# Kernel optimization log

Measured on AMD Instinct MI355X. Metric: run time of the kernel, lower is better.

The kernel has to match this reference:

```python
import jax, jax.numpy as jnp
import numpy as np
import math

VOCAB, E, CTX, DK, DH, H, HID, L = 50257, 768, 2048, 64, 64, 12, 3072, 2
B, S = 2, 2048
NEG_INF = -1e30


def _pos_encoding(seq_len, dim):
    pos = jnp.arange(seq_len, dtype=jnp.float32)[:, None]
    i = jnp.arange(dim, dtype=jnp.float32)[None, :]
    angle = pos / jnp.power(10000.0, 2.0 * i / dim)
    return jnp.where(jnp.arange(dim)[None, :] % 2 == 0, jnp.sin(angle), jnp.cos(angle))


def _layernorm(x, scale, bias, eps=1e-5):
    mu = jnp.mean(x, axis=-1, keepdims=True)
    var = jnp.var(x, axis=-1, keepdims=True)
    return (x - mu) * jax.lax.rsqrt(var + eps) * scale + bias


def setup_inputs() -> dict:
    key = jax.random.key(0)
    ks = jax.random.split(key, 10)
    s = 0.02  # init scale for stability
    return {
        "tokens": jax.random.randint(ks[0], (B, S), 0, VOCAB),
        "emb": jax.random.normal(ks[1], (VOCAB, E), jnp.float32) * s,
        "ln1_s": jnp.ones((L, E), jnp.float32),
        "ln1_b": jnp.zeros((L, E), jnp.float32),
        "Wq": jax.random.normal(ks[2], (L, H, E, DK), jnp.float32) * s,
        "bq": jnp.zeros((L, H, DK), jnp.float32),
        "Wk": jax.random.normal(ks[3], (L, H, E, DK), jnp.float32) * s,
        "bk": jnp.zeros((L, H, DK), jnp.float32),
        "Wv": jax.random.normal(ks[4], (L, H, E, DH), jnp.float32) * s,
        "bv": jnp.zeros((L, H, DH), jnp.float32),
        "ln2_s": jnp.ones((L, E), jnp.float32),
        "ln2_b": jnp.zeros((L, E), jnp.float32),
        "W1": jax.random.normal(ks[5], (L, E, HID), jnp.float32) * s,
        "b1": jnp.zeros((L, HID), jnp.float32),
        "W2": jax.random.normal(ks[6], (L, HID, E), jnp.float32) * s,
        "b2": jnp.zeros((L, E), jnp.float32),
        "Wout": jax.random.normal(ks[7], (E, VOCAB), jnp.float32) * s,
        "bout": jnp.zeros((VOCAB,), jnp.float32),
    }


def reference(tokens, emb, ln1_s, ln1_b, Wq, bq, Wk, bk, Wv, bv, ln2_s, ln2_b, W1, b1, W2, b2, Wout, bout):
    seq = tokens.shape[1]
    x = emb[tokens] + _pos_encoding(seq, E)  # [B,S,E]
    causal = jnp.triu(jnp.full((seq, seq), NEG_INF, jnp.float32), k=1)
    for l in range(Wq.shape[0]):
        # pre-norm on attention input; note residual adds to the NORMALIZED h (faithful to original)
        h = _layernorm(x, ln1_s[l], ln1_b[l])
        q = jnp.einsum('bse,hed->bhsd', h, Wq[l]) + bq[l][None, :, None, :]
        k = jnp.einsum('bse,hed->bhsd', h, Wk[l]) + bk[l][None, :, None, :]
        v = jnp.einsum('bse,hed->bhsd', h, Wv[l]) + bv[l][None, :, None, :]
        scores = jnp.einsum('bhsd,bhtd->bhst', q, k) / math.sqrt(DK) + causal
        w = jax.nn.softmax(scores, axis=-1)  # [B,H,S,S]
        o = jnp.einsum('bhst,bhtd->bhsd', w, v)  # [B,H,S,DH]
        o = jnp.transpose(o, (0, 2, 1, 3)).reshape(o.shape[0], seq, H * DH)  # concat heads
        x = h + o
        h2 = _layernorm(x, ln2_s[l], ln2_b[l])
        x = h2 + jnp.einsum('bsf,fe->bse', jax.nn.relu(jnp.einsum('bse,ef->bsf', h2, W1[l]) + b1[l]), W2[l]) + b2[l]
    logits = jnp.einsum('bse,ev->bsv', x, Wout) + bout  # training-mode output
    return logits
```

## Files before the change

kernel.cpp:

```cpp
#include <hip/hip_runtime.h>
#include <stdint.h>

#define DEV static __device__ __forceinline__

typedef unsigned short u16;
typedef __attribute__((ext_vector_type(8))) short short8;
typedef __attribute__((ext_vector_type(4))) float f32x4;

#define B_     2
#define S_     2048
#define E_     768
#define H_     12
#define L_     2
#define HID_   3072
#define VOCAB_ 50257
#define VPAD_  50432
#define M_     4096
#define NQKV_  2304

DEV u16 f2bf(float f) {
  union { float f; unsigned u; } x; x.f = f;
  unsigned r = x.u + 0x7fffu + ((x.u >> 16) & 1u);
  return (u16)(r >> 16);
}

DEV void gload16(const void* g, void* lds) {
  __builtin_amdgcn_global_load_lds(
      (const __attribute__((address_space(1))) unsigned int*)g,
      (__attribute__((address_space(3))) unsigned int*)lds, 16, 0, 0);
}

__global__ __launch_bounds__(256) void k_transp(
    const float* __restrict__ in, u16* __restrict__ out,
    int R, int Cin, long long ib1, long long ib2, long long ob1, long long ob2, int zdiv)
{
  __shared__ float t[32][33];
  const int z = blockIdx.z;
  const float* ib = in  + (size_t)(z / zdiv) * ib1 + (size_t)(z % zdiv) * ib2;
  u16*         ob = out + (size_t)(z / zdiv) * ob1 + (size_t)(z % zdiv) * ob2;
  const int c0 = blockIdx.x * 32, r0 = blockIdx.y * 32;
  const int tx = threadIdx.x, ty = threadIdx.y;
#pragma unroll
  for (int i = 0; i < 4; i++) {
    const int c = c0 + tx, r = r0 + ty + i * 8;
    t[ty + i * 8][tx] = (c < Cin) ? ib[(size_t)r * Cin + c] : 0.f;
  }
  __syncthreads();
#pragma unroll
  for (int i = 0; i < 4; i++) {
    const int orow = c0 + ty + i * 8;
    ob[(size_t)orow * R + r0 + tx] = f2bf(t[tx][ty + i * 8]);
  }
}

__global__ __launch_bounds__(256) void k_pack_bias(
    const float* __restrict__ bq, const float* __restrict__ bk,
    const float* __restrict__ bv, float* __restrict__ bqkv)
{
  const int i = blockIdx.x * 256 + threadIdx.x;
  if (i >= L_ * NQKV_) return;
  const int l = i / NQKV_, n = i % NQKV_;
  const float* s = (n < 768) ? bq : (n < 1536) ? bk : bv;
  bqkv[i] = s[l * 768 + (n % 768)];
}

__global__ __launch_bounds__(256) void k_embed(
    const int* __restrict__ tok, const float* __restrict__ emb, float* __restrict__ x)
{
  const int idx = blockIdx.x * 256 + threadIdx.x;
  const int e = idx % E_;
  const int row = idx / E_;
  const int s = row & (S_ - 1);
  const int t = tok[row];
  const float ang = (float)s * expf((float)e * (-2.0f / 768.f) * 9.210340371976184f);
  const float pe = (e & 1) ? cosf(ang) : sinf(ang);
  x[idx] = emb[(size_t)t * E_ + e] + pe;
}

__global__ __launch_bounds__(256) void k_ln(
    const float* __restrict__ xin, const float* __restrict__ sc,
    const float* __restrict__ bi, float* __restrict__ hout, u16* __restrict__ hb)
{
  const int row  = blockIdx.x * 4 + (threadIdx.x >> 6);
  const int lane = threadIdx.x & 63;
  const float* xr = xin + (size_t)row * E_;
  float v[12];
  float s = 0.f;
#pragma unroll
  for (int i = 0; i < 12; i++) { v[i] = xr[i * 64 + lane]; s += v[i]; }
#pragma unroll
  for (int o = 1; o < 64; o <<= 1) s += __shfl_xor(s, o);
  const float mu = s * (1.f / 768.f);
  float s2 = 0.f;
#pragma unroll
  for (int i = 0; i < 12; i++) { const float d = v[i] - mu; s2 += d * d; }
#pragma unroll
  for (int o = 1; o < 64; o <<= 1) s2 += __shfl_xor(s2, o);
  const float rs = rsqrtf(s2 * (1.f / 768.f) + 1e-5f);
#pragma unroll
  for (int i = 0; i < 12; i++) {
    const int c = i * 64 + lane;
    const float ov = (v[i] - mu) * rs * sc[c] + bi[c];
    hout[(size_t)row * E_ + c] = ov;
    hb[(size_t)row * E_ + c]   = f2bf(ov);
  }
}

template <int EPI>
__global__ __launch_bounds__(256) void k_gemm(
    const u16* __restrict__ A, const u16* __restrict__ Bt,
    const float* __restrict__ bias, const float* __restrict__ res,
    void* __restrict__ outp, u16* __restrict__ out2, int Mm, int Nn, int Kk)
{
  __shared__ __align__(16) u16 As[128 * 32];
  __shared__ __align__(16) u16 Bs[128 * 32];
  const int tid  = threadIdx.x;
  const int lane = tid & 63;
  const int wid  = tid >> 6;
  const int wr = wid >> 1, wc = wid & 1;
  const int m0 = blockIdx.y * 128, n0 = blockIdx.x * 128;

  const u16* Ab = A  + (size_t)m0 * Kk;
  const u16* Bb = Bt + (size_t)n0 * Kk;

  f32x4 acc[4][4];
#pragma unroll
  for (int i = 0; i < 4; i++)
#pragma unroll
    for (int j = 0; j < 4; j++) acc[i][j] = (f32x4){0.f, 0.f, 0.f, 0.f};

  const int c0 = tid, c1 = 256 + tid;
  const int a0row = c0 >> 2, a0k = (c0 & 3) * 8;
  const int a1row = c1 >> 2, a1k = (c1 & 3) * 8;
  const int nk = Kk >> 5;
  const int kg = (lane >> 4) * 8;
  const int arow = wr * 64 + (lane & 15);
  const int brow = wc * 64 + (lane & 15);

  for (int kt = 0; kt < nk; ++kt) {
    const int kof = kt * 32;
    __syncthreads();
    gload16(Ab + (size_t)a0row * Kk + kof + a0k, &As[c0 * 8]);
    gload16(Ab + (size_t)a1row * Kk + kof + a1k, &As[c1 * 8]);
    gload16(Bb + (size_t)a0row * Kk + kof + a0k, &Bs[c0 * 8]);
    gload16(Bb + (size_t)a1row * Kk + kof + a1k, &Bs[c1 * 8]);
    asm volatile("s_waitcnt vmcnt(0)" ::: "memory");
    __syncthreads();
    short8 af[4], bf[4];
#pragma unroll
    for (int i = 0; i < 4; i++) af[i] = *(const short8*)&As[(arow + i * 16) * 32 + kg];
#pragma unroll
    for (int i = 0; i < 4; i++) bf[i] = *(const short8*)&Bs[(brow + i * 16) * 32 + kg];
#pragma unroll
    for (int mi = 0; mi < 4; mi++)
#pragma unroll
      for (int ni = 0; ni < 4; ni++)
        acc[mi][ni] = __builtin_amdgcn_mfma_f32_16x16x32_bf16(af[mi], bf[ni], acc[mi][ni], 0, 0, 0);
  }

  const int colg = lane & 15;
  const int rowg = (lane >> 4) * 4;
#pragma unroll
  for (int mi = 0; mi < 4; mi++) {
#pragma unroll
    for (int ni = 0; ni < 4; ni++) {
      const int col = n0 + wc * 64 + ni * 16 + colg;
      const float bb = bias[col];
#pragma unroll
      for (int r = 0; r < 4; r++) {
        const int row = m0 + wr * 64 + mi * 16 + rowg + r;
        float v = acc[mi][ni][r] + bb;
        if (EPI == 0)      ((u16*)outp)[(size_t)row * Nn + col] = f2bf(v);
        else if (EPI == 1) ((u16*)outp)[(size_t)row * Nn + col] = f2bf(fmaxf(v, 0.f));
        else if (EPI == 2) ((float*)outp)[(size_t)row * Nn + col] = v + res[(size_t)row * Nn + col];
        else if (EPI == 4) {
          const float o = v + res[(size_t)row * Nn + col];
          ((float*)outp)[(size_t)row * Nn + col] = o;
          out2[(size_t)row * Nn + col] = f2bf(o);
        }
      }
    }
  }
}

__global__ __launch_bounds__(512, 2) void k_gemm256(
    const u16* __restrict__ A, const u16* __restrict__ Bt,
    const float* __restrict__ bias, float* __restrict__ out,
    int Nn, int Kk, int nreal, int mpx)
{
  __shared__ __align__(16) u16 As[2][256 * 64];
  __shared__ __align__(16) u16 Bs[2][256 * 64];

  const int id = blockIdx.x;
  const int xcd = id & 7;
  const int j = id >> 3;
  const int m0 = (xcd * mpx + (j % mpx)) * 256;
  const int n0 = (j / mpx) * 256;

  const int tid = threadIdx.x, lane = tid & 63, w = tid >> 6;
  const int wr = w >> 2, wcn = w & 3;
  const int l15 = lane & 15, ks = lane >> 4;

  const u16* Ab = A  + (size_t)m0 * Kk;
  const u16* Bb = Bt + (size_t)n0 * Kk;

  const int srow  = lane >> 3;
  const int sslot = ((lane & 7) ^ srow) * 8;
  const int wrow  = w * 8;

  f32x4 acc[8][4];
#pragma unroll
  for (int i = 0; i < 8; i++)
#pragma unroll
    for (int n = 0; n < 4; n++) acc[i][n] = (f32x4){0.f, 0.f, 0.f, 0.f};

  const int nk = Kk >> 6;

  auto stage = [&](int b, int ko) {
    gload16(Ab + (size_t)(wrow + srow) * Kk + ko + sslot,       &As[b][wrow * 64]);
    gload16(Ab + (size_t)(64 + wrow + srow) * Kk + ko + sslot,  &As[b][(64 + wrow) * 64]);
    gload16(Ab + (size_t)(128 + wrow + srow) * Kk + ko + sslot, &As[b][(128 + wrow) * 64]);
    gload16(Ab + (size_t)(192 + wrow + srow) * Kk + ko + sslot, &As[b][(192 + wrow) * 64]);
    gload16(Bb + (size_t)(wrow + srow) * Kk + ko + sslot,       &Bs[b][wrow * 64]);
    gload16(Bb + (size_t)(64 + wrow + srow) * Kk + ko + sslot,  &Bs[b][(64 + wrow) * 64]);
    gload16(Bb + (size_t)(128 + wrow + srow) * Kk + ko + sslot, &Bs[b][(128 + wrow) * 64]);
    gload16(Bb + (size_t)(192 + wrow + srow) * Kk + ko + sslot, &Bs[b][(192 + wrow) * 64]);
  };

  short8 af[4], bf[4];
  auto ldA = [&](int b, int fmh, int ksub) {
#pragma unroll
    for (int i = 0; i < 4; i++) {
      const int r = wr * 128 + fmh * 64 + i * 16 + l15;
      const int sl = ((ksub * 4 + ks) ^ (r & 7)) * 8;
      af[i] = *(const short8*)&As[b][r * 64 + sl];
    }
  };
  auto ldB = [&](int b, int ksub) {
#pragma unroll
    for (int n = 0; n < 4; n++) {
      const int r = wcn * 64 + n * 16 + l15;
      const int sl = ((ksub * 4 + ks) ^ (r & 7)) * 8;
      bf[n] = *(const short8*)&Bs[b][r * 64 + sl];
    }
  };
  auto mm = [&](int fmh) {
    __builtin_amdgcn_s_setprio(1);
#pragma unroll
    for (int i = 0; i < 4; i++)
#pragma unroll
      for (int n = 0; n < 4; n++)
        acc[fmh * 4 + i][n] =
            __builtin_amdgcn_mfma_f32_16x16x32_bf16(af[i], bf[n], acc[fmh * 4 + i][n], 0, 0, 0);
    __builtin_amdgcn_s_setprio(0);
  };

  stage(0, 0);
  if (nk > 1) {
    stage(1, 64);
    asm volatile("s_waitcnt vmcnt(8)" ::: "memory");
  } else {
    asm volatile("s_waitcnt vmcnt(0)" ::: "memory");
  }
  __builtin_amdgcn_s_barrier();

  for (int t = 0; t < nk; ++t) {
    const int cur = t & 1;
    ldA(cur, 0, 0); ldB(cur, 0); mm(0);
    ldA(cur, 1, 0); mm(1);
    ldA(cur, 0, 1); ldB(cur, 1); mm(0);
    ldA(cur, 1, 1); mm(1);
    __builtin_amdgcn_sched_barrier(0);
    __builtin_amdgcn_s_barrier();
    __builtin_amdgcn_sched_barrier(0);
    if (t + 2 < nk) {
      stage(cur, (t + 2) << 6);
      asm volatile("s_waitcnt vmcnt(8)" ::: "memory");
    } else if (t + 1 < nk) {
      asm volatile("s_waitcnt vmcnt(0)" ::: "memory");
    }
    __builtin_amdgcn_sched_barrier(0);
    __builtin_amdgcn_s_barrier();
    __builtin_amdgcn_sched_barrier(0);
  }

#pragma unroll
  for (int fm = 0; fm < 8; fm++) {
    const int row = m0 + wr * 128 + fm * 16 + ks * 4;
#pragma unroll
    for (int n = 0; n < 4; n++) {
      const int col = n0 + wcn * 64 + n * 16 + l15;
      if (col < nreal) {
        const float bb = bias[col];
#pragma unroll
        for (int r = 0; r < 4; r++)
          out[(size_t)(row + r) * nreal + col] = acc[fm][n][r] + bb;
      }
    }
  }
}

__global__ __launch_bounds__(256) void k_attn(
    const u16* __restrict__ qkv, const float* __restrict__ h, float* __restrict__ x)
{
  const int tid = threadIdx.x, lane = tid & 63, wid = tid >> 6;
  const int bh = blockIdx.y, b = bh / H_, hh = bh % H_;
  const int q0 = blockIdx.x * 64;
  const int qw = q0 + wid * 16;

  __shared__ __align__(16) u16 Ks[128 * 72];
  __shared__ __align__(16) u16 Vt[64 * 136];
  __shared__ __align__(16) u16 Ps[4][16 * 136];

  const size_t rowbase = (size_t)b * S_;
  const u16* qb = qkv + rowbase * NQKV_ + hh * 64;
  const u16* kb = qb + 768;
  const u16* vb = qb + 1536;

  const int l15 = lane & 15;
  const int ks  = lane >> 4;
  const int kg  = ks * 8;
  const int ks4 = ks * 4;

  short8 qf0, qf1;
  {
    const u16* g = qb + (size_t)(qw + l15) * NQKV_ + kg;
    qf0 = *(const short8*)g;
    qf1 = *(const short8*)(g + 32);
  }

  f32x4 ov[4];
#pragma unroll
  for (int i = 0; i < 4; i++) ov[i] = (f32x4){0.f, 0.f, 0.f, 0.f};
  float mr[4], lr[4];
#pragma unroll
  for (int r = 0; r < 4; r++) { mr[r] = -1e30f; lr[r] = 0.f; }

  const int srow = tid >> 3;
  const int sc8  = (tid & 7) * 8;
  const int g8   = tid & 7;
  const int nkt  = (q0 >> 7) + 1;

  for (int kt = 0; kt < nkt; ++kt) {
    const int kbase = kt << 7;
    __syncthreads();
#pragma unroll
    for (int pass = 0; pass < 4; ++pass) {
      const int r = srow + pass * 32;
      const size_t gr = (size_t)(kbase + r) * NQKV_;
      const uint4 kd = *(const uint4*)(kb + gr + sc8);
      *(uint4*)&Ks[r * 72 + sc8] = kd;
      const uint4 vd = *(const uint4*)(vb + gr + sc8);
      const u16* ve = (const u16*)&vd;
      const int sb = (((r >> 3) ^ g8) << 3) + (r & 7);
#pragma unroll
      for (int jj = 0; jj < 8; jj++) Vt[(sc8 + jj) * 136 + sb] = ve[jj];
    }
    __syncthreads();

    const bool last = (kt == nkt - 1);
    float p[8][4], mt[4];
#pragma unroll
    for (int r = 0; r < 4; r++) mt[r] = -1e30f;
#pragma unroll
    for (int ct = 0; ct < 8; ++ct) {
      f32x4 s = (f32x4){0.f, 0.f, 0.f, 0.f};
      const short8 kf0 = *(const short8*)&Ks[(ct * 16 + l15) * 72 + kg];
      const short8 kf1 = *(const short8*)&Ks[(ct * 16 + l15) * 72 + 32 + kg];
      s = __builtin_amdgcn_mfma_f32_16x16x32_bf16(qf0, kf0, s, 0, 0, 0);
      s = __builtin_amdgcn_mfma_f32_16x16x32_bf16(qf1, kf1, s, 0, 0, 0);
      const int kc = kbase + ct * 16 + l15;
#pragma unroll
      for (int r = 0; r < 4; r++) {
        float v = s[r] * 0.125f;
        if (last && kc > qw + ks4 + r) v = -1e30f;
        p[ct][r] = v;
        mt[r] = fmaxf(mt[r], v);
      }
    }
#pragma unroll
    for (int r = 0; r < 4; r++) {
#pragma unroll
      for (int off = 1; off < 16; off <<= 1) mt[r] = fmaxf(mt[r], __shfl_xor(mt[r], off));
    }
    float al[4], ps[4];
#pragma unroll
    for (int r = 0; r < 4; r++) {
      const float mn = fmaxf(mr[r], mt[r]);
      al[r] = __expf(mr[r] - mn);
      mr[r] = mn;
      ps[r] = 0.f;
    }
#pragma unroll
    for (int ct = 0; ct < 8; ++ct)
#pragma unroll
      for (int r = 0; r < 4; r++) {
        p[ct][r] = __expf(p[ct][r] - mr[r]);
        ps[r] += p[ct][r];
      }
#pragma unroll
    for (int r = 0; r < 4; r++) {
#pragma unroll
      for (int off = 1; off < 16; off <<= 1) ps[r] += __shfl_xor(ps[r], off);
      lr[r] = lr[r] * al[r] + ps[r];
    }
#pragma unroll
    for (int dt = 0; dt < 4; dt++)
#pragma unroll
      for (int r = 0; r < 4; r++) ov[dt][r] *= al[r];

    u16* pw = &Ps[wid][0];
#pragma unroll
    for (int ct = 0; ct < 8; ++ct)
#pragma unroll
      for (int r = 0; r < 4; r++)
        pw[(ks4 + r) * 136 + ct * 16 + l15] = f2bf(p[ct][r]);
#pragma unroll
    for (int c = 0; c < 4; ++c) {
      const short8 pa = *(const short8*)&pw[l15 * 136 + c * 32 + kg];
#pragma unroll
      for (int dt = 0; dt < 4; dt++) {
        const int d = dt * 16 + l15;
        const int sb = (((c * 4 + ks) ^ ((d >> 3) & 7)) << 3);
        const short8 vf = *(const short8*)&Vt[d * 136 + sb];
        ov[dt] = __builtin_amdgcn_mfma_f32_16x16x32_bf16(pa, vf, ov[dt], 0, 0, 0);
      }
    }
  }

#pragma unroll
  for (int dt = 0; dt < 4; dt++) {
#pragma unroll
    for (int r = 0; r < 4; r++) {
      const int qr = qw + ks4 + r;
      const int col = hh * 64 + dt * 16 + l15;
      const size_t idx = (rowbase + qr) * (size_t)E_ + col;
      x[idx] = h[idx] + ov[dt][r] / lr[r];
    }
  }
}

extern "C" void kernel_launch(void* const* d_in, const int* in_sizes, int n_in,
                              void* d_out, int out_size, void* d_ws, size_t ws_size,
                              hipStream_t stream)
{
  const int*   tok  = (const int*)  d_in[0];
  const float* emb  = (const float*)d_in[1];
  const float* ln1s = (const float*)d_in[2];
  const float* ln1b = (const float*)d_in[3];
  const float* Wq   = (const float*)d_in[4];
  const float* bq   = (const float*)d_in[5];
  const float* Wk   = (const float*)d_in[6];
  const float* bk   = (const float*)d_in[7];
  const float* Wv   = (const float*)d_in[8];
  const float* bv   = (const float*)d_in[9];
  const float* ln2s = (const float*)d_in[10];
  const float* ln2b = (const float*)d_in[11];
  const float* W1   = (const float*)d_in[12];
  const float* b1   = (const float*)d_in[13];
  const float* W2   = (const float*)d_in[14];
  const float* b2   = (const float*)d_in[15];
  const float* Wo   = (const float*)d_in[16];
  const float* bo   = (const float*)d_in[17];
  float* out = (float*)d_out;

  char* p = (char*)d_ws;
  float* xf    = (float*)p; p += (size_t)M_ * E_ * 4;
  float* hf    = (float*)p; p += (size_t)M_ * E_ * 4;
  u16*   hb    = (u16*)p;   p += (size_t)M_ * E_ * 2;
  u16*   xb    = (u16*)p;   p += (size_t)M_ * E_ * 2;
  u16*   midb  = (u16*)p;   p += (size_t)M_ * HID_ * 2;
  u16*   qkvb  = (u16*)p;   p += (size_t)M_ * NQKV_ * 2;
  u16*   Wqkvt = (u16*)p;   p += (size_t)L_ * NQKV_ * E_ * 2;
  u16*   W1t   = (u16*)p;   p += (size_t)L_ * HID_ * E_ * 2;
  u16*   W2t   = (u16*)p;   p += (size_t)L_ * E_ * HID_ * 2;
  u16*   Wot   = (u16*)p;   p += (size_t)VPAD_ * E_ * 2;
  float* bqkv  = (float*)p; p += (size_t)L_ * NQKV_ * 4;

  const dim3 tb32(32, 8, 1);
  k_transp<<<dim3(HID_ / 32, E_ / 32, L_), tb32, 0, stream>>>(
      W1, W1t, E_, HID_, (long long)E_ * HID_, 0, (long long)HID_ * E_, 0, 1);
  k_transp<<<dim3(E_ / 32, HID_ / 32, L_), tb32, 0, stream>>>(
      W2, W2t, HID_, E_, (long long)HID_ * E_, 0, (long long)E_ * HID_, 0, 1);
  k_transp<<<dim3(VPAD_ / 32, E_ / 32, 1), tb32, 0, stream>>>(
      Wo, Wot, E_, VOCAB_, 0, 0, 0, 0, 1);
  k_transp<<<dim3(2, E_ / 32, L_ * H_), tb32, 0, stream>>>(
      Wq, Wqkvt, E_, 64, (long long)H_ * E_ * 64, (long long)E_ * 64,
      (long long)NQKV_ * E_, 64LL * E_, H_);
  k_transp<<<dim3(2, E_ / 32, L_ * H_), tb32, 0, stream>>>(
      Wk, Wqkvt + 768 * E_, E_, 64, (long long)H_ * E_ * 64, (long long)E_ * 64,
      (long long)NQKV_ * E_, 64LL * E_, H_);
  k_transp<<<dim3(2, E_ / 32, L_ * H_), tb32, 0, stream>>>(
      Wv, Wqkvt + 1536 * E_, E_, 64, (long long)H_ * E_ * 64, (long long)E_ * 64,
      (long long)NQKV_ * E_, 64LL * E_, H_);
  k_pack_bias<<<18, 256, 0, stream>>>(bq, bk, bv, bqkv);
  k_embed<<<(M_ * E_) / 256, 256, 0, stream>>>(tok, emb, xf);

  for (int l = 0; l < L_; ++l) {
    k_ln<<<M_ / 4, 256, 0, stream>>>(xf, ln1s + l * E_, ln1b + l * E_, hf, hb);
    k_gemm<0><<<dim3(NQKV_ / 128, M_ / 128), 256, 0, stream>>>(
        hb, Wqkvt + (size_t)l * NQKV_ * E_, bqkv + l * NQKV_, nullptr, qkvb, nullptr,
        M_, NQKV_, E_);
    k_attn<<<dim3(S_ / 64, B_ * H_), 256, 0, stream>>>(qkvb, hf, xf);
    k_ln<<<M_ / 4, 256, 0, stream>>>(xf, ln2s + l * E_, ln2b + l * E_, hf, hb);
    k_gemm<1><<<dim3(HID_ / 128, M_ / 128), 256, 0, stream>>>(
        hb, W1t + (size_t)l * HID_ * E_, b1 + l * HID_, nullptr, midb, nullptr,
        M_, HID_, E_);
    if (l == L_ - 1) {
      k_gemm<4><<<dim3(E_ / 128, M_ / 128), 256, 0, stream>>>(
          midb, W2t + (size_t)l * E_ * HID_, b2 + l * E_, hf, xf, xb, M_, E_, HID_);
    } else {
      k_gemm<2><<<dim3(E_ / 128, M_ / 128), 256, 0, stream>>>(
          midb, W2t + (size_t)l * E_ * HID_, b2 + l * E_, hf, xf, nullptr, M_, E_, HID_);
    }
  }
  k_gemm256<<<dim3(8 * 2 * (VPAD_ / 256)), 512, 0, stream>>>(
      xb, Wot, bo, out, VPAD_, E_, VOCAB_, 2);
}
```

Before: 1.186 ms.

## Restructure vocab GEMM to 1024 threads with 64x64 warp tiles and K=32 stages

The output-projection GEMM now runs 16 waves per 256x256 tile instead of 8, so each wave owns a 64x64 sub-tile and half as many accumulators. The K step drops from 64 to 32, which halves shared memory per buffer, and the swizzle is rewritten for 32-element rows. The pipeline goes from two stages issued ahead to a simpler one-ahead double buffer. The aim is higher occupancy and more latency hiding, at the cost of more barriers per K and less register-level reuse of A and B fragments.

Result: slower. 1.298 ms (+9.5%).

```diff
diff --git a/kernel.cpp b/kernel.cpp
--- a/kernel.cpp
+++ b/kernel.cpp
@@ -183,13 +183,13 @@
   }
 }
 
-__global__ __launch_bounds__(512, 2) void k_gemm256(
+__global__ __launch_bounds__(1024, 4) void k_gemm256(
     const u16* __restrict__ A, const u16* __restrict__ Bt,
     const float* __restrict__ bias, float* __restrict__ out,
     int Nn, int Kk, int nreal, int mpx)
 {
-  __shared__ __align__(16) u16 As[2][256 * 64];
-  __shared__ __align__(16) u16 Bs[2][256 * 64];
+  __shared__ __align__(16) u16 As[2][256 * 32];
+  __shared__ __align__(16) u16 Bs[2][256 * 32];
 
   const int id = blockIdx.x;
   const int xcd = id & 7;
@@ -198,103 +198,83 @@
   const int n0 = (j / mpx) * 256;
 
   const int tid = threadIdx.x, lane = tid & 63, w = tid >> 6;
-  const int wr = w >> 2, wcn = w & 3;
+  const int wm = w >> 2, wn = w & 3;
   const int l15 = lane & 15, ks = lane >> 4;
 
   const u16* Ab = A  + (size_t)m0 * Kk;
   const u16* Bb = Bt + (size_t)n0 * Kk;
 
-  const int srow  = lane >> 3;
-  const int sslot = ((lane & 7) ^ srow) * 8;
-  const int wrow  = w * 8;
-
-  f32x4 acc[8][4];
-#pragma unroll
-  for (int i = 0; i < 8; i++)
+  const int rowc  = lane >> 2;
+  const int sslot = (((lane & 3) ^ ((lane >> 2) & 3) ^ ((lane >> 4) & 3))) * 8;
+  const size_t soff = (size_t)(w * 16 + rowc) * Kk + sslot;
+
+  f32x4 acc[4][4];
+#pragma unroll
+  for (int i = 0; i < 4; i++)
 #pragma unroll
     for (int n = 0; n < 4; n++) acc[i][n] = (f32x4){0.f, 0.f, 0.f, 0.f};
 
-  const int nk = Kk >> 6;
+  const int nk = Kk >> 5;
 
   auto stage = [&](int b, int ko) {
-    gload16(Ab + (size_t)(wrow + srow) * Kk + ko + sslot,       &As[b][wrow * 64]);
-    gload16(Ab + (size_t)(64 + wrow + srow) * Kk + ko + sslot,  &As[b][(64 + wrow) * 64]);
-    gload16(Ab + (size_t)(128 + wrow + srow) * Kk + ko + sslot, &As[b][(128 + wrow) * 64]);
-    gload16(Ab + (size_t)(192 + wrow + srow) * Kk + ko + sslot, &As[b][(192 + wrow) * 64]);
-    gload16(Bb + (size_t)(wrow + srow) * Kk + ko + sslot,       &Bs[b][wrow * 64]);
-    gload16(Bb + (size_t)(64 + wrow + srow) * Kk + ko + sslot,  &Bs[b][(64 + wrow) * 64]);
-    gload16(Bb + (size_t)(128 + wrow + srow) * Kk + ko + sslot, &Bs[b][(128 + wrow) * 64]);
-    gload16(Bb + (size_t)(192 + wrow + srow) * Kk + ko + sslot, &Bs[b][(192 + wrow) * 64]);
+    gload16(Ab + soff + ko, &As[b][w * 512]);
+    gload16(Bb + soff + ko, &Bs[b][w * 512]);
   };
 
-  short8 af[4], bf[4];
-  auto ldA = [&](int b, int fmh, int ksub) {
-#pragma unroll
-    for (int i = 0; i < 4; i++) {
-      const int r = wr * 128 + fmh * 64 + i * 16 + l15;
-      const int sl = ((ksub * 4 + ks) ^ (r & 7)) * 8;
-      af[i] = *(const short8*)&As[b][r * 64 + sl];
+  const int sl8 = ((ks ^ (l15 & 3) ^ ((l15 >> 2) & 3))) * 8;
+
+  short8 af, bf[4];
+  auto ldB = [&](int b) {
+#pragma unroll
+    for (int n = 0; n < 4; n++) {
+      const int r = wn * 64 + n * 16 + l15;
+      bf[n] = *(const short8*)&Bs[b][r * 32 + sl8];
     }
   };
-  auto ldB = [&](int b, int ksub) {
-#pragma unroll
-    for (int n = 0; n < 4; n++) {
-      const int r = wcn * 64 + n * 16 + l15;
-      const int sl = ((ksub * 4 + ks) ^ (r & 7)) * 8;
-      bf[n] = *(const short8*)&Bs[b][r * 64 + sl];
-    }
-  };
-  auto mm = [&](int fmh) {
-    __builtin_amdgcn_s_setprio(1);
-#pragma unroll
-    for (int i = 0; i < 4; i++)
-#pragma unroll
-      for (int n = 0; n < 4; n++)
-        acc[fmh * 4 + i][n] =
-            __builtin_amdgcn_mfma_f32_16x16x32_bf16(af[i], bf[n], acc[fmh * 4 + i][n], 0, 0, 0);
-    __builtin_amdgcn_s_setprio(0);
-  };
 
   stage(0, 0);
-  if (nk > 1) {
-    stage(1, 64);
-    asm volatile("s_waitcnt vmcnt(8)" ::: "memory");
-  } else {
-    asm volatile("s_waitcnt vmcnt(0)" ::: "memory");
-  }
-  __builtin_amdgcn_s_barrier();
 
   for (int t = 0; t < nk; ++t) {
     const int cur = t & 1;
-    ldA(cur, 0, 0); ldB(cur, 0); mm(0);
-    ldA(cur, 1, 0); mm(1);
-    ldA(cur, 0, 1); ldB(cur, 1); mm(0);
-    ldA(cur, 1, 1); mm(1);
+    if (t + 1 < nk) {
+      stage(cur ^ 1, (t + 1) * 32);
+      asm volatile("s_waitcnt vmcnt(2)" ::: "memory");
+    } else {
+      asm volatile("s_waitcnt vmcnt(0)" ::: "memory");
+    }
     __builtin_amdgcn_sched_barrier(0);
     __builtin_amdgcn_s_barrier();
     __builtin_amdgcn_sched_barrier(0);
-    if (t + 2 < nk) {
-      stage(cur, (t + 2) << 6);
-      asm volatile("s_waitcnt vmcnt(8)" ::: "memory");
-    } else if (t + 1 < nk) {
-      asm volatile("s_waitcnt vmcnt(0)" ::: "memory");
-    }
+
+    ldB(cur);
+#pragma unroll
+    for (int m = 0; m < 4; m++) {
+      const int r = wm * 64 + m * 16 + l15;
+      af = *(const short8*)&As[cur][r * 32 + sl8];
+      __builtin_amdgcn_s_setprio(1);
+#pragma unroll
+      for (int n = 0; n < 4; n++)
+        acc[m][n] = __builtin_amdgcn_mfma_f32_16x16x32_bf16(af, bf[n], acc[m][n], 0, 0, 0);
+      __builtin_amdgcn_s_setprio(0);
+    }
+
     __builtin_amdgcn_sched_barrier(0);
     __builtin_amdgcn_s_barrier();
     __builtin_amdgcn_sched_barrier(0);
   }
 
 #pragma unroll
-  for (int fm = 0; fm < 8; fm++) {
-    const int row = m0 + wr * 128 + fm * 16 + ks * 4;
+  for (int m = 0; m < 4; m++) {
 #pragma unroll
     for (int n = 0; n < 4; n++) {
-      const int col = n0 + wcn * 64 + n * 16 + l15;
+      const int col = n0 + wn * 64 + n * 16 + l15;
       if (col < nreal) {
         const float bb = bias[col];
 #pragma unroll
-        for (int r = 0; r < 4; r++)
-          out[(size_t)(row + r) * nreal + col] = acc[fm][n][r] + bb;
+        for (int r = 0; r < 4; r++) {
+          const int row = m0 + wm * 64 + m * 16 + ks * 4 + r;
+          out[(size_t)row * nreal + col] = acc[m][n][r] + bb;
+        }
       }
     }
   }
@@ -514,6 +494,6 @@
           midb, W2t + (size_t)l * E_ * HID_, b2 + l * E_, hf, xf, nullptr, M_, E_, HID_);
     }
   }
-  k_gemm256<<<dim3(8 * 2 * (VPAD_ / 256)), 512, 0, stream>>>(
+  k_gemm256<<<dim3(8 * 2 * (VPAD_ / 256)), 1024, 0, stream>>>(
       xb, Wot, bo, out, VPAD_, E_, VOCAB_, 2);
 }
```
